# Kernel optimization log

Hardware: AMD Instinct MI355X
Metric: run time of the kernel (lower is better)

## Reference

```python
import jax, jax.numpy as jnp
import numpy as np

B = 4096
UNITS = 1024
OUT_STEPS = 128
W_SCALE = 0.02  # keep gates out of hard saturation


def setup_inputs() -> dict:
    key = jax.random.key(0)
    k1, k2, k3, k4 = jax.random.split(key, 4)
    features = jax.random.normal(k1, (B, UNITS // 2), dtype=jnp.float32)
    kernel = jax.random.normal(k2, (1, 4 * UNITS), dtype=jnp.float32) * W_SCALE
    recurrent_kernel = jax.random.normal(k3, (UNITS, 4 * UNITS), dtype=jnp.float32) * W_SCALE
    bias = jnp.zeros((4 * UNITS,), dtype=jnp.float32)
    dense_w = jax.random.normal(k4, (UNITS, 1), dtype=jnp.float32) * W_SCALE
    dense_b = jnp.zeros((1,), dtype=jnp.float32)
    return {
        "features": features,
        "kernel": kernel,
        "recurrent_kernel": recurrent_kernel,
        "bias": bias,
        "dense_w": dense_w,
        "dense_b": dense_b,
    }


def reference(features, kernel, recurrent_kernel, bias, dense_w, dense_b):
    # State init: h = c = concat([features, features], axis=1) -> [B, UNITS]
    h0 = jnp.concatenate([features, features], axis=1)
    c0 = h0
    x0 = jnp.zeros((features.shape[0], 1), dtype=features.dtype)

    def step(carry, _):
        x, h, c = carry
        # Keras LSTMCell: gates ordered (i, f, g, o)
        z = x @ kernel + h @ recurrent_kernel + bias  # [B, 4*UNITS]
        zi, zf, zg, zo = jnp.split(z, 4, axis=1)
        i = jax.nn.sigmoid(zi)
        f = jax.nn.sigmoid(zf)
        g = jnp.tanh(zg)
        o = jax.nn.sigmoid(zo)
        c_new = f * c + i * g
        h_new = o * jnp.tanh(c_new)
        pred = h_new @ dense_w + dense_b  # [B, 1], fed back as next input
        return (pred, h_new, c_new), pred

    _, preds = jax.lax.scan(step, (x0, h0, c0), None, length=OUT_STEPS)
    # preds: [T, B, 1] -> [B, T, 1] (matches tf.stack + transpose [1,0,2])
    return jnp.transpose(preds, (1, 0, 2))
```

## Files before the change

kernel.cpp:

```cpp
#include <hip/hip_runtime.h>
#include <hip/hip_bf16.h>
#include <stdint.h>

#define BATCH 4096
#define UNITS 1024
#define NSTEP 128

typedef __attribute__((ext_vector_type(4))) float f32x4;
typedef __attribute__((ext_vector_type(8))) short s16x8;

__device__ __forceinline__ void gload16(const void* g, void* l) {
  __builtin_amdgcn_global_load_lds(
      (const __attribute__((address_space(1))) unsigned int*)g,
      (__attribute__((address_space(3))) unsigned int*)l, 16, 0, 0);
}

__device__ __forceinline__ void block_barrier() {
  asm volatile("" ::: "memory");
  __builtin_amdgcn_s_barrier();
  asm volatile("" ::: "memory");
}

__device__ __forceinline__ float fsigmoid(float x) {
  return 1.0f / (1.0f + __expf(-x));
}
__device__ __forceinline__ float ftanh(float x) {
  return 1.0f - 2.0f / (__expf(2.0f * x) + 1.0f);
}

__global__ void prep_weights(const float* __restrict__ R,
                             const float* __restrict__ ker,
                             const float* __restrict__ dw,
                             __hip_bfloat16* __restrict__ Rt0,
                             __hip_bfloat16* __restrict__ Rt1) {
  __shared__ float tile[32][33];
  __shared__ float dws[32];
  const int n0 = blockIdx.x * 32;
  const int k0 = blockIdx.y * 32;
  const int tx = threadIdx.x;
  const int ty = threadIdx.y;
#pragma unroll
  for (int i = 0; i < 4; ++i) {
    int k = ty + i * 8;
    tile[k][tx] = R[(size_t)(k0 + k) * 4096 + n0 + tx];
  }
  if (ty == 0) dws[tx] = dw[k0 + tx];
  __syncthreads();
#pragma unroll
  for (int i = 0; i < 4; ++i) {
    int n = ty + i * 8;
    float v = tile[tx][n];
    int gn = n0 + n, gk = k0 + tx;
    int g = gn >> 10, u = gn & 1023;
    int q = u >> 6, wc = (u >> 4) & 3, ul = u & 15;
    int np = q * 256 + wc * 64 + g * 16 + ul;
    size_t o = (size_t)np * 1024 + gk;
    Rt0[o] = __float2bfloat16(v);
    Rt1[o] = __float2bfloat16(v + dws[tx] * ker[gn]);
  }
}

__global__ void prep_state(const float* __restrict__ feat,
                           const float* __restrict__ bias,
                           const float* __restrict__ ker,
                           const float* __restrict__ db,
                           float* __restrict__ bias1,
                           __hip_bfloat16* __restrict__ hA,
                           float* __restrict__ c,
                           float* __restrict__ out) {
  const int total = BATCH * UNITS;
  const float dbv = db[0];
  for (int i = blockIdx.x * blockDim.x + threadIdx.x; i < total;
       i += gridDim.x * blockDim.x) {
    int b = i >> 10, u = i & 1023;
    float v = feat[b * 512 + (u & 511)];
    hA[i] = __float2bfloat16(v);
    c[i] = v;
    if (i < 4096) bias1[i] = bias[i] + dbv * ker[i];
    if (i < BATCH * NSTEP) out[i] = dbv;
  }
}

__global__ __launch_bounds__(512, 2) void lstm_step(
    const __hip_bfloat16* __restrict__ hin,
    const __hip_bfloat16* __restrict__ Bp,
    const float* __restrict__ biasv,
    float* __restrict__ c,
    __hip_bfloat16* __restrict__ hout,
    const float* __restrict__ dw,
    float* __restrict__ out, int t) {
  extern __shared__ char lds[];
  const int tid = threadIdx.x;
  const int lane = tid & 63;
  const int w = tid >> 6;
  const int l15 = lane & 15;
  const int lhi = lane >> 4;
  const int wr = w >> 2;
  const int wc = w & 3;

  const int bi = blockIdx.x;
  const int xcd = bi & 7, slot = bi >> 3;
  const int bx = (xcd & 3) * 4 + (slot & 3);
  const int by = (xcd >> 2) * 8 + (slot >> 2);

  const int ucol = by * 64 + wc * 16 + l15;
  const float dwv = dw[ucol];

  f32x4 acc[8][4];
#pragma unroll
  for (int g = 0; g < 4; ++g) {
    float bg = biasv[g * 1024 + ucol];
#pragma unroll
    for (int m = 0; m < 8; ++m) acc[m][g] = (f32x4){bg, bg, bg, bg};
  }

  const char* Asrc = (const char*)(hin + (size_t)bx * 256 * 1024);
  const char* Bsrc = (const char*)(Bp + (size_t)by * 256 * 1024);
  const int kb = ((lane & 7) * 16) ^ ((lane >> 3) << 4);
  const int swz = (l15 & 7) << 4;

  auto STAGE = [&](int kt) {
    const int k0b = kt * 128;
    char* Ad = lds + (kt & 1) * 32768;
    char* Bd = lds + 65536 + (kt & 1) * 32768;
#pragma unroll
    for (int j = 0; j < 4; ++j) {
      int r = (w * 4 + j) * 8 + (lane >> 3);
      gload16(Asrc + (size_t)r * 2048 + k0b + kb, Ad + (w * 4 + j) * 1024);
      gload16(Bsrc + (size_t)r * 2048 + k0b + kb, Bd + (w * 4 + j) * 1024);
    }
  };

  STAGE(0);
  STAGE(1);
  asm volatile("s_waitcnt vmcnt(8)" ::: "memory");
  block_barrier();

  for (int kt = 0; kt < 16; ++kt) {
    const char* Ab = lds + (kt & 1) * 32768;
    const char* Bb = lds + 65536 + (kt & 1) * 32768;
    s16x8 a0[8], b0[4];
#pragma unroll
    for (int m = 0; m < 8; ++m) {
      int row = wr * 128 + m * 16 + l15;
      a0[m] = *(const s16x8*)(Ab + row * 128 + ((lhi * 16) ^ swz));
    }
#pragma unroll
    for (int g = 0; g < 4; ++g) {
      int srow = wc * 64 + g * 16 + l15;
      b0[g] = *(const s16x8*)(Bb + srow * 128 + ((lhi * 16) ^ swz));
    }
    __builtin_amdgcn_s_setprio(1);
#pragma unroll
    for (int m = 0; m < 8; ++m)
#pragma unroll
      for (int g = 0; g < 4; ++g)
        acc[m][g] = __builtin_amdgcn_mfma_f32_16x16x32_bf16(a0[m], b0[g],
                                                            acc[m][g], 0, 0, 0);
    __builtin_amdgcn_s_setprio(0);
    s16x8 a1[8], b1[4];
#pragma unroll
    for (int m = 0; m < 8; ++m) {
      int row = wr * 128 + m * 16 + l15;
      a1[m] = *(const s16x8*)(Ab + row * 128 + ((64 + lhi * 16) ^ swz));
    }
#pragma unroll
    for (int g = 0; g < 4; ++g) {
      int srow = wc * 64 + g * 16 + l15;
      b1[g] = *(const s16x8*)(Bb + srow * 128 + ((64 + lhi * 16) ^ swz));
    }
    asm volatile("s_waitcnt lgkmcnt(0)" ::: "memory");
    __builtin_amdgcn_sched_barrier(0);
    block_barrier();
    if (kt < 14) STAGE(kt + 2);
    __builtin_amdgcn_s_setprio(1);
#pragma unroll
    for (int m = 0; m < 8; ++m)
#pragma unroll
      for (int g = 0; g < 4; ++g)
        acc[m][g] = __builtin_amdgcn_mfma_f32_16x16x32_bf16(a1[m], b1[g],
                                                            acc[m][g], 0, 0, 0);
    __builtin_amdgcn_s_setprio(0);
    if (kt < 14) asm volatile("s_waitcnt vmcnt(8)" ::: "memory");
    else         asm volatile("s_waitcnt vmcnt(0)" ::: "memory");
    block_barrier();
  }

#pragma unroll
  for (int m = 0; m < 8; ++m) {
#pragma unroll
    for (int j = 0; j < 4; ++j) {
      int b = bx * 256 + wr * 128 + m * 16 + lhi * 4 + j;
      size_t ci = (size_t)b * 1024 + ucol;
      float zi = acc[m][0][j], zf = acc[m][1][j];
      float zg = acc[m][2][j], zo = acc[m][3][j];
      float ig = fsigmoid(zi), fg = fsigmoid(zf);
      float gg = ftanh(zg), og = fsigmoid(zo);
      float cn = fg * c[ci] + ig * gg;
      c[ci] = cn;
      float hn = og * ftanh(cn);
      hout[ci] = __float2bfloat16(hn);
      float p = hn * dwv;
      p += __shfl_xor(p, 1);
      p += __shfl_xor(p, 2);
      p += __shfl_xor(p, 4);
      p += __shfl_xor(p, 8);
      if (l15 == 0) atomicAdd(&out[(size_t)b * NSTEP + t], p);
    }
  }
}

extern "C" void kernel_launch(void* const* d_in, const int* in_sizes, int n_in,
                              void* d_out, int out_size, void* d_ws, size_t ws_size,
                              hipStream_t stream) {
  const float* feat = (const float*)d_in[0];
  const float* ker  = (const float*)d_in[1];
  const float* R    = (const float*)d_in[2];
  const float* bias = (const float*)d_in[3];
  const float* dw   = (const float*)d_in[4];
  const float* db   = (const float*)d_in[5];
  float* out = (float*)d_out;

  char* ws = (char*)d_ws;
  const size_t MB = 1024 * 1024;
  __hip_bfloat16* Rt0 = (__hip_bfloat16*)(ws);
  __hip_bfloat16* Rt1 = (__hip_bfloat16*)(ws + 8 * MB);
  float* bias1 = (float*)(ws + 16 * MB);
  __hip_bfloat16* hA = (__hip_bfloat16*)(ws + 16 * MB + 65536);
  __hip_bfloat16* hB = (__hip_bfloat16*)(ws + 24 * MB + 65536);
  float* cbuf = (float*)(ws + 32 * MB + 65536);

  hipFuncSetAttribute((const void*)lstm_step,
                      hipFuncAttributeMaxDynamicSharedMemorySize, 131072);

  prep_weights<<<dim3(128, 32), dim3(32, 8), 0, stream>>>(R, ker, dw, Rt0, Rt1);
  prep_state<<<4096, 256, 0, stream>>>(feat, bias, ker, db, bias1, hA, cbuf, out);

  for (int t = 0; t < NSTEP; ++t) {
    const __hip_bfloat16* hin = (t & 1) ? hB : hA;
    __hip_bfloat16* hout = (t & 1) ? hA : hB;
    lstm_step<<<256, 512, 131072, stream>>>(
        hin, (t == 0) ? Rt0 : Rt1, (t == 0) ? bias : bias1, cbuf, hout, dw, out, t);
  }
}
```

Baseline: 6.437 ms.

## Switch GEMM mainloop to triple-buffered 32-wide K tiles with one barrier

Restructures the recurrent GEMM K-loop from 16 double-buffered 64-wide K tiles with two barriers per iteration to 32 triple-buffered 32-wide K tiles with a single barrier per iteration. It also changes the LDS swizzle and layout, and issues the next tile's global-to-LDS loads between the fragment reads. The aim is to cut barrier stalls and overlap loads with MFMA work, and LDS use drops from 128KB to 96KB. The cost is more loop iterations and more wait points per K, plus the risk that the new swizzle causes bank conflicts or indexing bugs.

```diff
diff --git a/kernel.cpp b/kernel.cpp
--- a/kernel.cpp
+++ b/kernel.cpp
@@ -116,74 +116,74 @@
 
   const char* Asrc = (const char*)(hin + (size_t)bx * 256 * 1024);
   const char* Bsrc = (const char*)(Bp + (size_t)by * 256 * 1024);
-  const int kb = ((lane & 7) * 16) ^ ((lane >> 3) << 4);
-  const int swz = (l15 & 7) << 4;
-
-  auto STAGE = [&](int kt) {
-    const int k0b = kt * 128;
-    char* Ad = lds + (kt & 1) * 32768;
-    char* Bd = lds + 65536 + (kt & 1) * 32768;
-#pragma unroll
-    for (int j = 0; j < 4; ++j) {
-      int r = (w * 4 + j) * 8 + (lane >> 3);
-      gload16(Asrc + (size_t)r * 2048 + k0b + kb, Ad + (w * 4 + j) * 1024);
-      gload16(Bsrc + (size_t)r * 2048 + k0b + kb, Bd + (w * 4 + j) * 1024);
+  const int ksl = (((lane & 3) ^ ((lane >> 2) & 3)) << 4);
+  const int sl = ((lhi ^ (l15 & 3)) << 4);
+  const int vA = wr * 8192 + l15 * 64 + sl;
+  const int vB = wc * 4096 + l15 * 64 + sl;
+
+  auto STAGE_A = [&](int kt, char* dst) {
+#pragma unroll
+    for (int i = 0; i < 2; ++i) {
+      int row = w * 32 + i * 16 + (lane >> 2);
+      gload16(Asrc + (size_t)row * 2048 + kt * 64 + ksl,
+              dst + (w * 2 + i) * 1024);
     }
   };
-
-  STAGE(0);
-  STAGE(1);
-  asm volatile("s_waitcnt vmcnt(8)" ::: "memory");
-  block_barrier();
-
-  for (int kt = 0; kt < 16; ++kt) {
-    const char* Ab = lds + (kt & 1) * 32768;
-    const char* Bb = lds + 65536 + (kt & 1) * 32768;
-    s16x8 a0[8], b0[4];
-#pragma unroll
-    for (int m = 0; m < 8; ++m) {
-      int row = wr * 128 + m * 16 + l15;
-      a0[m] = *(const s16x8*)(Ab + row * 128 + ((lhi * 16) ^ swz));
+  auto STAGE_B = [&](int kt, char* dst) {
+#pragma unroll
+    for (int i = 0; i < 2; ++i) {
+      int row = w * 32 + i * 16 + (lane >> 2);
+      gload16(Bsrc + (size_t)row * 2048 + kt * 64 + ksl,
+              dst + 16384 + (w * 2 + i) * 1024);
     }
-#pragma unroll
-    for (int g = 0; g < 4; ++g) {
-      int srow = wc * 64 + g * 16 + l15;
-      b0[g] = *(const s16x8*)(Bb + srow * 128 + ((lhi * 16) ^ swz));
-    }
+  };
+
+  STAGE_A(0, lds);          STAGE_B(0, lds);
+  STAGE_A(1, lds + 32768);  STAGE_B(1, lds + 32768);
+
+  int j2 = 0, js = 2;
+  for (int kt = 0; kt < 32; ++kt) {
+    if (kt < 31) asm volatile("s_waitcnt vmcnt(4)" ::: "memory");
+    else         asm volatile("s_waitcnt vmcnt(0)" ::: "memory");
+    block_barrier();
+    const char* Ab = lds + j2 * 32768;
+    const char* Bb = Ab + 16384;
+    char* Sd = lds + js * 32768;
+
+    s16x8 a0[4], a1[4], b0[4];
+#pragma unroll
+    for (int m = 0; m < 4; ++m) a0[m] = *(const s16x8*)(Ab + vA + m * 1024);
+#pragma unroll
+    for (int g = 0; g < 4; ++g) b0[g] = *(const s16x8*)(Bb + vB + g * 1024);
+    if (kt < 30) STAGE_A(kt + 2, Sd);
+#pragma unroll
+    for (int m = 0; m < 4; ++m) a1[m] = *(const s16x8*)(Ab + vA + (m + 4) * 1024);
+    if (kt < 30) STAGE_B(kt + 2, Sd);
+
+    asm volatile("s_waitcnt lgkmcnt(4)" ::: "memory");
+    __builtin_amdgcn_sched_barrier(0);
     __builtin_amdgcn_s_setprio(1);
 #pragma unroll
-    for (int m = 0; m < 8; ++m)
+    for (int m = 0; m < 4; ++m)
 #pragma unroll
       for (int g = 0; g < 4; ++g)
         acc[m][g] = __builtin_amdgcn_mfma_f32_16x16x32_bf16(a0[m], b0[g],
                                                             acc[m][g], 0, 0, 0);
     __builtin_amdgcn_s_setprio(0);
-    s16x8 a1[8], b1[4];
-#pragma unroll
-    for (int m = 0; m < 8; ++m) {
-      int row = wr * 128 + m * 16 + l15;
-      a1[m] = *(const s16x8*)(Ab + row * 128 + ((64 + lhi * 16) ^ swz));
-    }
-#pragma unroll
-    for (int g = 0; g < 4; ++g) {
-      int srow = wc * 64 + g * 16 + l15;
-      b1[g] = *(const s16x8*)(Bb + srow * 128 + ((64 + lhi * 16) ^ swz));
-    }
+
     asm volatile("s_waitcnt lgkmcnt(0)" ::: "memory");
     __builtin_amdgcn_sched_barrier(0);
-    block_barrier();
-    if (kt < 14) STAGE(kt + 2);
     __builtin_amdgcn_s_setprio(1);
 #pragma unroll
-    for (int m = 0; m < 8; ++m)
+    for (int m = 0; m < 4; ++m)
 #pragma unroll
       for (int g = 0; g < 4; ++g)
-        acc[m][g] = __builtin_amdgcn_mfma_f32_16x16x32_bf16(a1[m], b1[g],
-                                                            acc[m][g], 0, 0, 0);
+        acc[m + 4][g] = __builtin_amdgcn_mfma_f32_16x16x32_bf16(a1[m], b0[g],
+                                                                acc[m + 4][g], 0, 0, 0);
     __builtin_amdgcn_s_setprio(0);
-    if (kt < 14) asm volatile("s_waitcnt vmcnt(8)" ::: "memory");
-    else         asm volatile("s_waitcnt vmcnt(0)" ::: "memory");
-    block_barrier();
+
+    j2 = (j2 == 2) ? 0 : j2 + 1;
+    js = (js == 2) ? 0 : js + 1;
   }
 
 #pragma unroll
@@ -231,7 +231,7 @@
   float* cbuf = (float*)(ws + 32 * MB + 65536);
 
   hipFuncSetAttribute((const void*)lstm_step,
-                      hipFuncAttributeMaxDynamicSharedMemorySize, 131072);
+                      hipFuncAttributeMaxDynamicSharedMemorySize, 98304);
 
   prep_weights<<<dim3(128, 32), dim3(32, 8), 0, stream>>>(R, ker, dw, Rt0, Rt1);
   prep_state<<<4096, 256, 0, stream>>>(feat, bias, ker, db, bias1, hA, cbuf, out);
@@ -239,7 +239,7 @@
   for (int t = 0; t < NSTEP; ++t) {
     const __hip_bfloat16* hin = (t & 1) ? hB : hA;
     __hip_bfloat16* hout = (t & 1) ? hA : hB;
-    lstm_step<<<256, 512, 131072, stream>>>(
+    lstm_step<<<256, 512, 98304, stream>>>(
         hin, (t == 0) ? Rt0 : Rt1, (t == 0) ? bias : bias1, cbuf, hout, dw, out, t);
   }
 }
```

Result: no change. 6.489 ms (+0.8%).

## Restructure GEMM main loop into quadrant-staged 8-wave ping-pong pipeline

Applied to the files above, without the earlier changes.

Reorders the permuted recurrent weight layout so each wave's gate tiles split into low (i,f) and high (g,o) halves, and remaps the A rows per wave into two 128-row halves. The K loop now loads one 128-wide K tile per iteration into a full 64 KB double buffer and computes four quadrant sub-GEMMs in turn. Each global prefetch of the next tile's quarter is issued between them, with finer vmcnt waits and barriers. The aim is to overlap LDS reads, global loads and MFMA more evenly and to keep fewer fragments live, at the cost of more barriers per iteration.

```diff
diff --git a/kernel.cpp b/kernel.cpp
--- a/kernel.cpp
+++ b/kernel.cpp
@@ -53,7 +53,7 @@
     int gn = n0 + n, gk = k0 + tx;
     int g = gn >> 10, u = gn & 1023;
     int q = u >> 6, wc = (u >> 4) & 3, ul = u & 15;
-    int np = q * 256 + wc * 64 + g * 16 + ul;
+    int np = q * 256 + (g >> 1) * 128 + wc * 32 + (g & 1) * 16 + ul;
     size_t o = (size_t)np * 1024 + gk;
     Rt0[o] = __float2bfloat16(v);
     Rt1[o] = __float2bfloat16(v + dws[tx] * ker[gn]);
@@ -116,81 +116,128 @@
 
   const char* Asrc = (const char*)(hin + (size_t)bx * 256 * 1024);
   const char* Bsrc = (const char*)(Bp + (size_t)by * 256 * 1024);
-  const int kb = ((lane & 7) * 16) ^ ((lane >> 3) << 4);
   const int swz = (l15 & 7) << 4;
 
-  auto STAGE = [&](int kt) {
-    const int k0b = kt * 128;
-    char* Ad = lds + (kt & 1) * 32768;
-    char* Bd = lds + 65536 + (kt & 1) * 32768;
-#pragma unroll
-    for (int j = 0; j < 4; ++j) {
-      int r = (w * 4 + j) * 8 + (lane >> 3);
-      gload16(Asrc + (size_t)r * 2048 + k0b + kb, Ad + (w * 4 + j) * 1024);
-      gload16(Bsrc + (size_t)r * 2048 + k0b + kb, Bd + (w * 4 + j) * 1024);
+  auto STAGE = [&](const char* src, int rowoff, int kt, char* dstbase) {
+#pragma unroll
+    for (int i = 0; i < 2; ++i) {
+      int chunk = i * 512 + tid;
+      int row = chunk >> 3, s = chunk & 7;
+      gload16(src + (size_t)(rowoff + row) * 2048 + kt * 128 +
+                  ((s * 16) ^ ((row & 7) << 4)),
+              dstbase + i * 8192 + w * 1024 + lane * 16);
     }
   };
 
-  STAGE(0);
-  STAGE(1);
-  asm volatile("s_waitcnt vmcnt(8)" ::: "memory");
-  block_barrier();
+  STAGE(Asrc, 0,   0, lds);
+  STAGE(Bsrc, 0,   0, lds + 32768);
+  STAGE(Bsrc, 128, 0, lds + 32768 + 16384);
+  STAGE(Asrc, 128, 0, lds + 16384);
 
   for (int kt = 0; kt < 16; ++kt) {
-    const char* Ab = lds + (kt & 1) * 32768;
-    const char* Bb = lds + 65536 + (kt & 1) * 32768;
-    s16x8 a0[8], b0[4];
-#pragma unroll
-    for (int m = 0; m < 8; ++m) {
-      int row = wr * 128 + m * 16 + l15;
-      a0[m] = *(const s16x8*)(Ab + row * 128 + ((lhi * 16) ^ swz));
-    }
-#pragma unroll
-    for (int g = 0; g < 4; ++g) {
-      int srow = wc * 64 + g * 16 + l15;
-      b0[g] = *(const s16x8*)(Bb + srow * 128 + ((lhi * 16) ^ swz));
-    }
-    __builtin_amdgcn_s_setprio(1);
-#pragma unroll
-    for (int m = 0; m < 8; ++m)
-#pragma unroll
-      for (int g = 0; g < 4; ++g)
-        acc[m][g] = __builtin_amdgcn_mfma_f32_16x16x32_bf16(a0[m], b0[g],
-                                                            acc[m][g], 0, 0, 0);
-    __builtin_amdgcn_s_setprio(0);
-    s16x8 a1[8], b1[4];
-#pragma unroll
-    for (int m = 0; m < 8; ++m) {
-      int row = wr * 128 + m * 16 + l15;
-      a1[m] = *(const s16x8*)(Ab + row * 128 + ((64 + lhi * 16) ^ swz));
-    }
-#pragma unroll
-    for (int g = 0; g < 4; ++g) {
-      int srow = wc * 64 + g * 16 + l15;
-      b1[g] = *(const s16x8*)(Bb + srow * 128 + ((64 + lhi * 16) ^ swz));
-    }
+    const char* Ab = lds + (kt & 1) * 65536;
+    const char* Bb = Ab + 32768;
+    char* Sd = lds + ((kt + 1) & 1) * 65536;
+    const bool pf = (kt < 15);
+
+    s16x8 al[4][2], bl[2][2], bh[2][2], ah[4][2];
+
+    asm volatile("s_waitcnt vmcnt(4)" ::: "memory");
+    block_barrier();
+#pragma unroll
+    for (int m = 0; m < 4; ++m) {
+      int row = wr * 64 + m * 16 + l15;
+#pragma unroll
+      for (int kk = 0; kk < 2; ++kk)
+        al[m][kk] = *(const s16x8*)(Ab + row * 128 + ((kk * 64 + lhi * 16) ^ swz));
+    }
+#pragma unroll
+    for (int g = 0; g < 2; ++g) {
+      int row = wc * 32 + g * 16 + l15;
+#pragma unroll
+      for (int kk = 0; kk < 2; ++kk)
+        bl[g][kk] = *(const s16x8*)(Bb + row * 128 + ((kk * 64 + lhi * 16) ^ swz));
+    }
+    if (pf) STAGE(Asrc, 0, kt + 1, Sd);
     asm volatile("s_waitcnt lgkmcnt(0)" ::: "memory");
     __builtin_amdgcn_sched_barrier(0);
+    __builtin_amdgcn_s_setprio(1);
+#pragma unroll
+    for (int m = 0; m < 4; ++m)
+#pragma unroll
+      for (int g = 0; g < 2; ++g)
+#pragma unroll
+        for (int kk = 0; kk < 2; ++kk)
+          acc[m][g] = __builtin_amdgcn_mfma_f32_16x16x32_bf16(
+              al[m][kk], bl[g][kk], acc[m][g], 0, 0, 0);
+    __builtin_amdgcn_s_setprio(0);
+
+    if (pf) asm volatile("s_waitcnt vmcnt(4)" ::: "memory");
+    else    asm volatile("s_waitcnt vmcnt(2)" ::: "memory");
     block_barrier();
-    if (kt < 14) STAGE(kt + 2);
-    __builtin_amdgcn_s_setprio(1);
-#pragma unroll
-    for (int m = 0; m < 8; ++m)
-#pragma unroll
-      for (int g = 0; g < 4; ++g)
-        acc[m][g] = __builtin_amdgcn_mfma_f32_16x16x32_bf16(a1[m], b1[g],
-                                                            acc[m][g], 0, 0, 0);
-    __builtin_amdgcn_s_setprio(0);
-    if (kt < 14) asm volatile("s_waitcnt vmcnt(8)" ::: "memory");
-    else         asm volatile("s_waitcnt vmcnt(0)" ::: "memory");
+#pragma unroll
+    for (int g = 0; g < 2; ++g) {
+      int row = 128 + wc * 32 + g * 16 + l15;
+#pragma unroll
+      for (int kk = 0; kk < 2; ++kk)
+        bh[g][kk] = *(const s16x8*)(Bb + row * 128 + ((kk * 64 + lhi * 16) ^ swz));
+    }
+    if (pf) STAGE(Bsrc, 0, kt + 1, Sd + 32768);
+    asm volatile("s_waitcnt lgkmcnt(0)" ::: "memory");
+    __builtin_amdgcn_sched_barrier(0);
+    __builtin_amdgcn_s_setprio(1);
+#pragma unroll
+    for (int m = 0; m < 4; ++m)
+#pragma unroll
+      for (int g = 0; g < 2; ++g)
+#pragma unroll
+        for (int kk = 0; kk < 2; ++kk)
+          acc[m][g + 2] = __builtin_amdgcn_mfma_f32_16x16x32_bf16(
+              al[m][kk], bh[g][kk], acc[m][g + 2], 0, 0, 0);
+    __builtin_amdgcn_s_setprio(0);
+
+    if (pf) asm volatile("s_waitcnt vmcnt(4)" ::: "memory");
+    else    asm volatile("s_waitcnt vmcnt(0)" ::: "memory");
     block_barrier();
+#pragma unroll
+    for (int m = 0; m < 4; ++m) {
+      int row = 128 + wr * 64 + m * 16 + l15;
+#pragma unroll
+      for (int kk = 0; kk < 2; ++kk)
+        ah[m][kk] = *(const s16x8*)(Ab + row * 128 + ((kk * 64 + lhi * 16) ^ swz));
+    }
+    if (pf) STAGE(Bsrc, 128, kt + 1, Sd + 32768 + 16384);
+    asm volatile("s_waitcnt lgkmcnt(0)" ::: "memory");
+    __builtin_amdgcn_sched_barrier(0);
+    __builtin_amdgcn_s_setprio(1);
+#pragma unroll
+    for (int m = 0; m < 4; ++m)
+#pragma unroll
+      for (int g = 0; g < 2; ++g)
+#pragma unroll
+        for (int kk = 0; kk < 2; ++kk)
+          acc[m + 4][g + 2] = __builtin_amdgcn_mfma_f32_16x16x32_bf16(
+              ah[m][kk], bh[g][kk], acc[m + 4][g + 2], 0, 0, 0);
+    __builtin_amdgcn_s_setprio(0);
+
+    if (pf) STAGE(Asrc, 128, kt + 1, Sd + 16384);
+    __builtin_amdgcn_s_setprio(1);
+#pragma unroll
+    for (int m = 0; m < 4; ++m)
+#pragma unroll
+      for (int g = 0; g < 2; ++g)
+#pragma unroll
+        for (int kk = 0; kk < 2; ++kk)
+          acc[m + 4][g] = __builtin_amdgcn_mfma_f32_16x16x32_bf16(
+              ah[m][kk], bl[g][kk], acc[m + 4][g], 0, 0, 0);
+    __builtin_amdgcn_s_setprio(0);
   }
 
 #pragma unroll
   for (int m = 0; m < 8; ++m) {
 #pragma unroll
     for (int j = 0; j < 4; ++j) {
-      int b = bx * 256 + wr * 128 + m * 16 + lhi * 4 + j;
+      int b = bx * 256 + (m >> 2) * 128 + wr * 64 + (m & 3) * 16 + lhi * 4 + j;
       size_t ci = (size_t)b * 1024 + ucol;
       float zi = acc[m][0][j], zf = acc[m][1][j];
       float zg = acc[m][2][j], zo = acc[m][3][j];
```

Result: faster. 6.112 ms (-5.1%).
